# Performance work log

Hardware: AMD Instinct MI355X
Metric: run time of the kernel (lower is better)

## Reference

```python
import jax, jax.numpy as jnp
import numpy as np

N_NODES = 50000
N_EDGES = 800000
IN_CH = 128
HID = 128
OUT_CH = 10
N_GRAPHS = 64
BN_EPS = 1e-5


def _lin_init(k, fan_in, fan_out):
    k1, k2 = jax.random.split(k)
    s = 1.0 / np.sqrt(fan_in)
    W = jax.random.uniform(k1, (fan_in, fan_out), minval=-s, maxval=s, dtype=jnp.float32)
    b = jax.random.uniform(k2, (fan_out,), minval=-s, maxval=s, dtype=jnp.float32)
    return W, b


def setup_inputs() -> dict:
    key = jax.random.key(0)
    ks = jax.random.split(key, 12)
    x = jax.random.normal(ks[0], (N_NODES, IN_CH), dtype=jnp.float32)
    edge_index = jax.random.randint(ks[1], (2, N_EDGES), 0, N_NODES, dtype=jnp.int32)
    batch = jnp.sort(jax.random.randint(ks[2], (N_NODES,), 0, N_GRAPHS, dtype=jnp.int32))
    Wb0, bb0 = _lin_init(ks[3], IN_CH, HID)
    Wb1, bb1 = _lin_init(ks[4], HID, HID)
    Wa0, ba0 = _lin_init(ks[5], HID, HID)
    Wa1, ba1 = _lin_init(ks[6], HID, HID)
    Wa2, ba2 = _lin_init(ks[7], HID, HID)
    Wh0, bh0 = _lin_init(ks[8], HID, HID)
    Wh1, bh1 = _lin_init(ks[9], HID, HID)
    Wh2, bh2 = _lin_init(ks[10], HID, OUT_CH)
    ones = jnp.ones((HID,), jnp.float32)
    zeros = jnp.zeros((HID,), jnp.float32)
    return {
        'x': x, 'edge_index': edge_index, 'batch': batch, 'num_graphs': N_GRAPHS,
        'Wb0': Wb0, 'bb0': bb0, 'gb0': ones, 'betab0': zeros, 'Wb1': Wb1, 'bb1': bb1,
        'Wa0': Wa0, 'ba0': ba0, 'ga0': ones, 'bea0': zeros,
        'Wa1': Wa1, 'ba1': ba1, 'ga1': ones, 'bea1': zeros,
        'Wa2': Wa2, 'ba2': ba2,
        'Wh0': Wh0, 'bh0': bh0, 'Wh1': Wh1, 'bh1': bh1, 'Wh2': Wh2, 'bh2': bh2,
    }


def _gcn_edges(edge_index, n):
    # add self-loops, symmetric deg^{-1/2} normalization (PyG GCNConv default)
    loop = jnp.arange(n, dtype=edge_index.dtype)
    src = jnp.concatenate([edge_index[0], loop])
    dst = jnp.concatenate([edge_index[1], loop])
    deg = jax.ops.segment_sum(jnp.ones_like(dst, dtype=jnp.float32), dst, num_segments=n)
    dinv = jnp.where(deg > 0, jax.lax.rsqrt(deg), 0.0)
    return src, dst, dinv[src] * dinv[dst]


def _conv(h, W, b, src, dst, ew, n):
    hw = h @ W  # [N, F_out]
    agg = jax.ops.segment_sum(hw[src] * ew[:, None], dst, num_segments=n)
    return agg + b


def _bn(h, g, b):
    # BatchNorm1d with track_running_stats=False -> always batch statistics
    mean = jnp.mean(h, axis=0)
    var = jnp.var(h, axis=0)
    return g * (h - mean) * jax.lax.rsqrt(var + BN_EPS) + b


def _gelu(h):
    return jax.nn.gelu(h, approximate=False)


def reference(x, edge_index, batch, num_graphs,
              Wb0, bb0, gb0, betab0, Wb1, bb1,
              Wa0, ba0, ga0, bea0, Wa1, ba1, ga1, bea1, Wa2, ba2,
              Wh0, bh0, Wh1, bh1, Wh2, bh2):
    n = x.shape[0]
    src, dst, ew = _gcn_edges(edge_index, n)
    # GCN stack before (2 layers): conv -> bn -> gelu -> conv
    h = _conv(x, Wb0, bb0, src, dst, ew, n)
    h = _gelu(_bn(h, gb0, betab0))
    h = _conv(h, Wb1, bb1, src, dst, ew, n)
    # GCN stack after (3 layers)
    h = _conv(h, Wa0, ba0, src, dst, ew, n)
    h = _gelu(_bn(h, ga0, bea0))
    h = _conv(h, Wa1, ba1, src, dst, ew, n)
    h = _gelu(_bn(h, ga1, bea1))
    h = _conv(h, Wa2, ba2, src, dst, ew, n)
    # global mean pool per graph
    sums = jax.ops.segment_sum(h, batch, num_segments=num_graphs)
    cnt = jax.ops.segment_sum(jnp.ones((n,), jnp.float32), batch, num_segments=num_graphs)
    pooled = sums / jnp.maximum(cnt, 1.0)[:, None]
    # MLP head (dropout is identity in eval)
    y = _gelu(pooled @ Wh0 + bh0)
    y = _gelu(y @ Wh1 + bh1)
    return y @ Wh2 + bh2
```

## Files before the change

### kernel.cpp

```cpp
#include <hip/hip_runtime.h>
#include <math.h>

#define NN 50000
#define NE 800000
#define CH 128
#define NG 64
#define BN_EPS 1e-5f
#define POOL_CHUNK 64
#define BKT_SHIFT 9
#define NBKT ((NN + 511) >> 9)
#define PTILE 2048
#define CAP 16384

typedef short bfrag8 __attribute__((ext_vector_type(8)));
typedef float facc4 __attribute__((ext_vector_type(4)));

__device__ __forceinline__ float gelu_f(float x) {
    return 0.5f * x * (1.0f + erff(x * 0.70710678118654752440f));
}

__device__ __forceinline__ unsigned int f2bf(float f) {
    unsigned int u = __float_as_uint(f);
    return (u + 0x7FFFu + ((u >> 16) & 1u)) >> 16;
}
__device__ __forceinline__ unsigned int pack_bf2(float lo, float hi) {
    return (f2bf(hi) << 16) | f2bf(lo);
}
__device__ __forceinline__ float bf_lo(unsigned int v) { return __uint_as_float(v << 16); }
__device__ __forceinline__ float bf_hi(unsigned int v) { return __uint_as_float(v & 0xFFFF0000u); }

__global__ __launch_bounds__(256) void part_k(const int* __restrict__ ei,
                                              int* __restrict__ btail,
                                              unsigned long long* __restrict__ part) {
    __shared__ int lh[NBKT];
    __shared__ int gbase[NBKT];
    int t = threadIdx.x;
    int base = blockIdx.x * PTILE;
    if (t < NBKT) lh[t] = 0;
    __syncthreads();
    int s[8], d[8], rk[8];
    #pragma unroll
    for (int i = 0; i < 8; ++i) {
        int e = base + i * 256 + t;
        if (e < NE) {
            s[i] = ei[e];
            d[i] = ei[NE + e];
            rk[i] = atomicAdd(&lh[d[i] >> BKT_SHIFT], 1);
        }
    }
    __syncthreads();
    if (t < NBKT && lh[t]) gbase[t] = t * CAP + atomicAdd(&btail[t], lh[t]);
    __syncthreads();
    #pragma unroll
    for (int i = 0; i < 8; ++i) {
        int e = base + i * 256 + t;
        if (e < NE) {
            int b = d[i] >> BKT_SHIFT;
            part[gbase[b] + rk[i]] =
                ((unsigned long long)(unsigned int)d[i] << 32) | (unsigned int)s[i];
        }
    }
}

__global__ __launch_bounds__(256) void cscat2_k(const unsigned long long* __restrict__ part,
                                                const int* __restrict__ btail,
                                                int* __restrict__ row_ptr,
                                                int* __restrict__ row_cnt,
                                                float* __restrict__ dinv,
                                                int* __restrict__ csr_src) {
    __shared__ int cnt_l[512];
    __shared__ int off_l[512];
    __shared__ int psc[256];
    int b = blockIdx.x;
    int n0 = b << BKT_SHIFT;
    int t = threadIdx.x;
    cnt_l[t] = 0;
    cnt_l[t + 256] = 0;
    __syncthreads();
    int e0 = b * CAP, e1 = e0 + btail[b];
    for (int e = e0 + t; e < e1; e += 256) {
        int d = (int)(part[e] >> 32);
        atomicAdd(&cnt_l[d - n0], 1);
    }
    __syncthreads();
    int c0 = cnt_l[2 * t], c1 = cnt_l[2 * t + 1];
    psc[t] = c0 + c1;
    __syncthreads();
    for (int off = 1; off < 256; off <<= 1) {
        int a = (t >= off) ? psc[t - off] : 0;
        __syncthreads();
        psc[t] += a;
        __syncthreads();
    }
    int excl = (t == 0) ? 0 : psc[t - 1];
    off_l[2 * t] = excl;
    off_l[2 * t + 1] = excl + c0;
    #pragma unroll
    for (int k = 0; k < 2; ++k) {
        int ln = 2 * t + k;
        int n = n0 + ln;
        if (n < NN) {
            int c = (k == 0) ? c0 : c1;
            row_ptr[n] = e0 + off_l[ln];
            row_cnt[n] = c;
            dinv[n] = rsqrtf((float)c + 1.0f);
        }
    }
    __syncthreads();
    cnt_l[t] = 0;
    cnt_l[t + 256] = 0;
    __syncthreads();
    for (int e = e0 + t; e < e1; e += 256) {
        unsigned long long p = part[e];
        int s = (int)(unsigned int)p;
        int ld = (int)(p >> 32) - n0;
        int pos = e0 + off_l[ld] + atomicAdd(&cnt_l[ld], 1);
        csr_src[pos] = s;
    }
}

__global__ __launch_bounds__(256) void wconv_all_k(const float* __restrict__ W0,
                                                   const float* __restrict__ W1,
                                                   const float* __restrict__ W2,
                                                   const float* __restrict__ W3,
                                                   const float* __restrict__ W4,
                                                   unsigned short* __restrict__ wf) {
    int which = blockIdx.x >> 3;
    int u = (blockIdx.x & 7) * 256 + threadIdx.x;
    const float* W = (which == 0) ? W0 : (which == 1) ? W1 : (which == 2) ? W2
                   : (which == 3) ? W3 : W4;
    unsigned short* dst_wf = wf + (size_t)which * 16384;
    int nt = u >> 8, kc = (u >> 6) & 3, l = u & 63;
    int kbase = kc * 32 + (l >> 4) * 8;
    int n = nt * 16 + (l & 15);
    unsigned int p[4];
    #pragma unroll
    for (int jj = 0; jj < 4; ++jj) {
        float a = W[(kbase + 2 * jj) * 128 + n];
        float b = W[(kbase + 2 * jj + 1) * 128 + n];
        p[jj] = pack_bf2(a, b);
    }
    *(uint4*)(dst_wf + (size_t)u * 8) = make_uint4(p[0], p[1], p[2], p[3]);
}

__device__ __forceinline__ void gemm_core(unsigned short* Alds, unsigned short* Wlds,
                                          const unsigned short* wfrag, int tid,
                                          int row0, unsigned int* out16) {
    #pragma unroll
    for (int i = 0; i < 8; ++i) {
        int linear = tid + i * 256;
        ((uint4*)Wlds)[linear] = ((const uint4*)wfrag)[linear];
    }
    __syncthreads();

    const int w = tid >> 6;
    const int l = tid & 63;
    const int quad = l >> 4;
    const int m = l & 15;

    facc4 acc[8];
    #pragma unroll
    for (int nt = 0; nt < 8; ++nt) acc[nt] = (facc4){0.f, 0.f, 0.f, 0.f};

    #pragma unroll
    for (int kc = 0; kc < 4; ++kc) {
        bfrag8 a = *((const bfrag8*)(Alds + ((size_t)((w * 4 + kc) * 64 + l)) * 8));
        #pragma unroll
        for (int nt = 0; nt < 8; ++nt) {
            bfrag8 b = *((const bfrag8*)(Wlds + ((size_t)((nt * 4 + kc) * 64 + l)) * 8));
            acc[nt] = __builtin_amdgcn_mfma_f32_16x16x32_bf16(a, b, acc[nt], 0, 0, 0);
        }
    }

    #pragma unroll
    for (int nt = 0; nt < 8; ++nt) {
        #pragma unroll
        for (int r = 0; r < 4; ++r) {
            int row = row0 + w * 16 + quad * 4 + r;
            if (row < NN)
                ((unsigned short*)out16)[(size_t)row * 128 + nt * 16 + m] =
                    (unsigned short)f2bf(acc[nt][r]);
        }
    }
}

__global__ __launch_bounds__(256) void gemm_f32_k(const float* __restrict__ A,
                                                  const unsigned short* __restrict__ wfrag,
                                                  unsigned int* __restrict__ out16) {
    __shared__ unsigned short Alds[8192];
    __shared__ unsigned short Wlds[16384];
    const int tid = threadIdx.x;
    const int row0 = blockIdx.x * 64;
    #pragma unroll
    for (int i = 0; i < 4; ++i) {
        int linear = tid + i * 256;
        int r = linear >> 4;
        int g = linear & 15;
        float4 v0 = make_float4(0.f, 0.f, 0.f, 0.f);
        float4 v1 = make_float4(0.f, 0.f, 0.f, 0.f);
        if (row0 + r < NN) {
            const float4* src = (const float4*)&A[(size_t)(row0 + r) * 128 + g * 8];
            v0 = src[0];
            v1 = src[1];
        }
        int unit = (((r >> 4) * 4 + (g >> 2)) * 64) + ((g & 3) * 16) + (r & 15);
        *(uint4*)(Alds + (size_t)unit * 8) =
            make_uint4(pack_bf2(v0.x, v0.y), pack_bf2(v0.z, v0.w),
                       pack_bf2(v1.x, v1.y), pack_bf2(v1.z, v1.w));
    }
    gemm_core(Alds, Wlds, wfrag, tid, row0, out16);
}

__global__ __launch_bounds__(256) void gemm_bf16_k(const unsigned int* __restrict__ h16,
                                                   const unsigned short* __restrict__ wfrag,
                                                   const float* __restrict__ ss,
                                                   unsigned int* __restrict__ out16) {
    __shared__ unsigned short Alds[8192];
    __shared__ unsigned short Wlds[16384];
    const int tid = threadIdx.x;
    const int row0 = blockIdx.x * 64;
    #pragma unroll
    for (int i = 0; i < 4; ++i) {
        int linear = tid + i * 256;
        int r = linear >> 4;
        int g = linear & 15;
        uint4 v = make_uint4(0u, 0u, 0u, 0u);
        if (row0 + r < NN)
            v = ((const uint4*)h16)[(size_t)(row0 + r) * 16 + g];
        if (ss) {
            float4 sc0 = ((const float4*)ss)[g * 2];
            float4 sh0 = ((const float4*)ss)[32 + g * 2];
            float4 sc1 = ((const float4*)ss)[g * 2 + 1];
            float4 sh1 = ((const float4*)ss)[32 + g * 2 + 1];
            float f0 = gelu_f(bf_lo(v.x) * sc0.x + sh0.x);
            float f1 = gelu_f(bf_hi(v.x) * sc0.y + sh0.y);
            float f2 = gelu_f(bf_lo(v.y) * sc0.z + sh0.z);
            float f3 = gelu_f(bf_hi(v.y) * sc0.w + sh0.w);
            float f4 = gelu_f(bf_lo(v.z) * sc1.x + sh1.x);
            float f5 = gelu_f(bf_hi(v.z) * sc1.y + sh1.y);
            float f6 = gelu_f(bf_lo(v.w) * sc1.z + sh1.z);
            float f7 = gelu_f(bf_hi(v.w) * sc1.w + sh1.w);
            v = make_uint4(pack_bf2(f0, f1), pack_bf2(f2, f3),
                           pack_bf2(f4, f5), pack_bf2(f6, f7));
        }
        int unit = (((r >> 4) * 4 + (g >> 2)) * 64) + ((g & 3) * 16) + (r & 15);
        *(uint4*)(Alds + (size_t)unit * 8) = v;
    }
    gemm_core(Alds, Wlds, wfrag, tid, row0, out16);
}

__global__ __launch_bounds__(256) void csr_agg_k(const int* __restrict__ row_ptr,
                                                 const int* __restrict__ row_cnt,
                                                 const int* __restrict__ csr_src,
                                                 const unsigned int* __restrict__ hw16,
                                                 const float* __restrict__ bias,
                                                 const float* __restrict__ dinv,
                                                 unsigned int* __restrict__ out16) {
    int node = (blockIdx.x * 256 + threadIdx.x) >> 6;
    if (node >= NN) return;
    int lane = threadIdx.x & 63;

    float di = dinv[node];
    float sw = di * di;
    float2 b = ((const float2*)bias)[lane];
    unsigned int hs = hw16[(size_t)node * 64 + lane];
    float selfx = b.x + bf_lo(hs) * sw;
    float selfy = b.y + bf_hi(hs) * sw;

    float a0x = 0.f, a0y = 0.f, a1x = 0.f, a1y = 0.f;
    float a2x = 0.f, a2y = 0.f, a3x = 0.f, a3y = 0.f;

    int j = row_ptr[node];
    int j1 = j + row_cnt[node];
    for (; j + 7 < j1; j += 8) {
        int s[8];
        #pragma unroll
        for (int k = 0; k < 8; ++k) s[k] = csr_src[j + k];
        float w[8];
        #pragma unroll
        for (int k = 0; k < 8; ++k) w[k] = dinv[s[k]];
        unsigned int v[8];
        #pragma unroll
        for (int k = 0; k < 8; ++k) v[k] = hw16[(size_t)s[k] * 64 + lane];
        a0x += bf_lo(v[0]) * w[0] + bf_lo(v[1]) * w[1];
        a0y += bf_hi(v[0]) * w[0] + bf_hi(v[1]) * w[1];
        a1x += bf_lo(v[2]) * w[2] + bf_lo(v[3]) * w[3];
        a1y += bf_hi(v[2]) * w[2] + bf_hi(v[3]) * w[3];
        a2x += bf_lo(v[4]) * w[4] + bf_lo(v[5]) * w[5];
        a2y += bf_hi(v[4]) * w[4] + bf_hi(v[5]) * w[5];
        a3x += bf_lo(v[6]) * w[6] + bf_lo(v[7]) * w[7];
        a3y += bf_hi(v[6]) * w[6] + bf_hi(v[7]) * w[7];
    }
    for (; j + 1 < j1; j += 2) {
        int s0 = csr_src[j], s1 = csr_src[j + 1];
        float w0 = dinv[s0], w1 = dinv[s1];
        unsigned int v0 = hw16[(size_t)s0 * 64 + lane];
        unsigned int v1 = hw16[(size_t)s1 * 64 + lane];
        a0x += bf_lo(v0) * w0 + bf_lo(v1) * w1;
        a0y += bf_hi(v0) * w0 + bf_hi(v1) * w1;
    }
    if (j < j1) {
        int s = csr_src[j];
        float w = dinv[s];
        unsigned int v = hw16[(size_t)s * 64 + lane];
        a0x += bf_lo(v) * w;
        a0y += bf_hi(v) * w;
    }
    float ox = selfx + di * ((a0x + a1x) + (a2x + a3x));
    float oy = selfy + di * ((a0y + a1y) + (a2y + a3y));
    out16[(size_t)node * 64 + lane] = pack_bf2(ox, oy);
}

__global__ __launch_bounds__(256) void bn_stats_k(const unsigned int* __restrict__ h16,
                                                  float* __restrict__ sums,
                                                  int* __restrict__ counter,
                                                  const float* __restrict__ g,
                                                  const float* __restrict__ beta,
                                                  float* __restrict__ ssout) {
    int t = threadIdx.x;
    int cp = t & 63;
    int quad = t >> 6;
    float s0 = 0.f, q0 = 0.f, s1 = 0.f, q1 = 0.f;
    int r0 = blockIdx.x * 128 + quad;
    #pragma unroll 4
    for (int i = 0; i < 32; ++i) {
        int r = r0 + i * 4;
        if (r < NN) {
            unsigned int v = h16[(size_t)r * 64 + cp];
            float f0 = bf_lo(v), f1 = bf_hi(v);
            s0 += f0; q0 += f0 * f0;
            s1 += f1; q1 += f1 * f1;
        }
    }
    __shared__ float A0[256], A1[256], A2[256], A3[256];
    A0[t] = s0; A1[t] = q0; A2[t] = s1; A3[t] = q1;
    __syncthreads();
    if (t < 64) {
        float ts0 = A0[t] + A0[64 + t] + A0[128 + t] + A0[192 + t];
        float tq0 = A1[t] + A1[64 + t] + A1[128 + t] + A1[192 + t];
        float ts1 = A2[t] + A2[64 + t] + A2[128 + t] + A2[192 + t];
        float tq1 = A3[t] + A3[64 + t] + A3[128 + t] + A3[192 + t];
        atomicAdd(&sums[2 * t], ts0);
        atomicAdd(&sums[2 * t + 1], ts1);
        atomicAdd(&sums[128 + 2 * t], tq0);
        atomicAdd(&sums[129 + 2 * t], tq1);
    }
    __threadfence();
    __syncthreads();
    __shared__ int isLast;
    if (t == 0) isLast = (atomicAdd(counter, 1) == (int)gridDim.x - 1);
    __syncthreads();
    if (isLast) {
        if (t < 128) {
            float sv = atomicAdd(&sums[t], 0.f);
            float qv = atomicAdd(&sums[128 + t], 0.f);
            float mean = sv * (1.0f / NN);
            float var = qv * (1.0f / NN) - mean * mean;
            float sc = g[t] * rsqrtf(var + BN_EPS);
            ssout[t] = sc;
            ssout[128 + t] = beta[t] - mean * sc;
            sums[t] = 0.f;
            sums[128 + t] = 0.f;
        }
        if (t == 0) *counter = 0;
    }
}

__global__ __launch_bounds__(128) void pool_sum_k(const unsigned int* __restrict__ h16,
                                                  const int* __restrict__ batch,
                                                  float* __restrict__ sums) {
    int r0 = blockIdx.x * POOL_CHUNK;
    int r1 = min(r0 + POOL_CHUNK, NN);
    if (r0 >= NN) return;
    int c = threadIdx.x;
    int cp = c >> 1, hi = c & 1;
    float acc = 0.f;
    int g = batch[r0];
    for (int r = r0; r < r1; ++r) {
        int gr = batch[r];
        if (gr != g) {
            atomicAdd(&sums[g * 128 + c], acc);
            acc = 0.f;
            g = gr;
        }
        unsigned int v = h16[(size_t)r * 64 + cp];
        acc += hi ? bf_hi(v) : bf_lo(v);
    }
    atomicAdd(&sums[g * 128 + c], acc);
}

__device__ __forceinline__ int lower_bound_dev(const int* __restrict__ a, int n, int key) {
    int lo = 0, hi = n;
    while (lo < hi) {
        int mid = (lo + hi) >> 1;
        if (a[mid] < key) lo = mid + 1; else hi = mid;
    }
    return lo;
}

__global__ __launch_bounds__(128) void head_k(const float* __restrict__ psum,
                                              const int* __restrict__ batch,
                                              const float* __restrict__ W0, const float* __restrict__ b0,
                                              const float* __restrict__ W1, const float* __restrict__ b1,
                                              const float* __restrict__ W2, const float* __restrict__ b2,
                                              float* __restrict__ out) {
    __shared__ float r0[128], r1[128];
    int g = blockIdx.x, t = threadIdx.x;
    int a = lower_bound_dev(batch, NN, g);
    int b = lower_bound_dev(batch, NN, g + 1);
    float inv = 1.0f / fmaxf((float)(b - a), 1.0f);
    r0[t] = psum[g * 128 + t] * inv;
    __syncthreads();
    float acc = b0[t];
    for (int k = 0; k < 128; ++k) acc += r0[k] * W0[k * 128 + t];
    r1[t] = gelu_f(acc);
    __syncthreads();
    acc = b1[t];
    for (int k = 0; k < 128; ++k) acc += r1[k] * W1[k * 128 + t];
    float y = gelu_f(acc);
    __syncthreads();
    r0[t] = y;
    __syncthreads();
    if (t < 10) {
        acc = b2[t];
        for (int k = 0; k < 128; ++k) acc += r0[k] * W2[k * 10 + t];
        out[g * 10 + t] = acc;
    }
}

extern "C" void kernel_launch(void* const* d_in, const int* in_sizes, int n_in,
                              void* d_out, int out_size, void* d_ws, size_t ws_size,
                              hipStream_t stream) {
    const float* x      = (const float*)d_in[0];
    const int*   ei     = (const int*)d_in[1];
    const int*   batch  = (const int*)d_in[2];
    const float* Wb0    = (const float*)d_in[4];
    const float* bb0    = (const float*)d_in[5];
    const float* gb0    = (const float*)d_in[6];
    const float* betab0 = (const float*)d_in[7];
    const float* Wb1    = (const float*)d_in[8];
    const float* bb1    = (const float*)d_in[9];
    const float* Wa0    = (const float*)d_in[10];
    const float* ba0    = (const float*)d_in[11];
    const float* ga0    = (const float*)d_in[12];
    const float* bea0   = (const float*)d_in[13];
    const float* Wa1    = (const float*)d_in[14];
    const float* ba1    = (const float*)d_in[15];
    const float* ga1    = (const float*)d_in[16];
    const float* bea1   = (const float*)d_in[17];
    const float* Wa2    = (const float*)d_in[18];
    const float* ba2    = (const float*)d_in[19];
    const float* Wh0    = (const float*)d_in[20];
    const float* bh0    = (const float*)d_in[21];
    const float* Wh1    = (const float*)d_in[22];
    const float* bh1    = (const float*)d_in[23];
    const float* Wh2    = (const float*)d_in[24];
    const float* bh2    = (const float*)d_in[25];
    float* out = (float*)d_out;

    char* ws = (char*)d_ws;
    unsigned int* hw16 = (unsigned int*)ws;             ws += (size_t)NN * 64 * 4;
    unsigned int* hB   = (unsigned int*)ws;             ws += (size_t)NN * 64 * 4;
    unsigned int* hC   = (unsigned int*)ws;             ws += (size_t)NN * 64 * 4;
    float* dinv    = (float*)ws;                        ws += (size_t)NN * 4;
    int*   row_ptr = (int*)ws;                          ws += (size_t)(NN + 4) * 4;
    int*   row_cnt = (int*)ws;                          ws += (size_t)NN * 4;
    int*   csr_src = (int*)ws;                          ws += (size_t)NBKT * CAP * 4;
    unsigned long long* part = (unsigned long long*)ws; ws += (size_t)NBKT * CAP * 8;
    unsigned short* wf = (unsigned short*)ws;           ws += (size_t)5 * 16384 * 2;
    float* ssbuf   = (float*)ws;                        ws += 256 * 4;
    char* zbase = ws;
    int*   btail   = (int*)ws;                          ws += 128 * 4;
    float* bnsums  = (float*)ws;                        ws += 256 * 4;
    int*   bncnt   = (int*)ws;                          ws += 4 * 4;
    float* psum    = (float*)ws;                        ws += (size_t)NG * CH * 4;
    size_t zbytes = (size_t)(ws - zbase);

    unsigned short* wfb0 = wf;
    unsigned short* wfb1 = wf + 16384;
    unsigned short* wfa0 = wf + 2 * 16384;
    unsigned short* wfa1 = wf + 3 * 16384;
    unsigned short* wfa2 = wf + 4 * 16384;

    hipMemsetAsync(zbase, 0, zbytes, stream);
    wconv_all_k<<<40, 256, 0, stream>>>(Wb0, Wb1, Wa0, Wa1, Wa2, wf);

    part_k<<<(NE + PTILE - 1) / PTILE, 256, 0, stream>>>(ei, btail, part);
    cscat2_k<<<NBKT, 256, 0, stream>>>(part, btail, row_ptr, row_cnt, dinv, csr_src);

    auto agg = [&](const float* b, unsigned int* o) {
        csr_agg_k<<<(NN * 64 + 255) / 256, 256, 0, stream>>>(row_ptr, row_cnt, csr_src,
                                                             hw16, b, dinv, o);
    };
    auto bn_stats = [&](const unsigned int* h, const float* g, const float* beta) {
        bn_stats_k<<<(NN + 127) / 128, 256, 0, stream>>>(h, bnsums, bncnt, g, beta, ssbuf);
    };

    gemm_f32_k<<<(NN + 63) / 64, 256, 0, stream>>>(x, wfb0, hw16);
    agg(bb0, hB);
    bn_stats(hB, gb0, betab0);
    gemm_bf16_k<<<(NN + 63) / 64, 256, 0, stream>>>(hB, wfb1, ssbuf, hw16);
    agg(bb1, hC);
    gemm_bf16_k<<<(NN + 63) / 64, 256, 0, stream>>>(hC, wfa0, nullptr, hw16);
    agg(ba0, hB);
    bn_stats(hB, ga0, bea0);
    gemm_bf16_k<<<(NN + 63) / 64, 256, 0, stream>>>(hB, wfa1, ssbuf, hw16);
    agg(ba1, hC);
    bn_stats(hC, ga1, bea1);
    gemm_bf16_k<<<(NN + 63) / 64, 256, 0, stream>>>(hC, wfa2, ssbuf, hw16);
    agg(ba2, hB);

    pool_sum_k<<<(NN + POOL_CHUNK - 1) / POOL_CHUNK, 128, 0, stream>>>(hB, batch, psum);
    head_k<<<NG, 128, 0, stream>>>(psum, batch, Wh0, bh0, Wh1, bh1, Wh2, bh2, out);
}
```

Measured before the change: 592.4 us.

## Fuse BatchNorm statistics into CSR aggregation with grid-stride waves

The aggregation kernel becomes a grid-stride loop over nodes using a fixed number of blocks, and accumulates per-channel sum and sum-of-squares of its fp32 outputs, reduced in shared memory and atomically added to a global buffer. The separate BN stats kernel that re-read the bf16 activations is replaced by a tiny one-block finalize kernel. This removes one full pass over the activation tensor per BN layer, at the cost of a fixed grid that may load-balance worse across irregular node degrees. Statistics are now computed from unrounded fp32 values rather than the stored bf16 values.

```diff
diff --git a/kernel.cpp b/kernel.cpp
--- a/kernel.cpp
+++ b/kernel.cpp
@@ -11,6 +11,7 @@
 #define NBKT ((NN + 511) >> 9)
 #define PTILE 2048
 #define CAP 16384
+#define AGG_BLOCKS 2048
 
 typedef short bfrag8 __attribute__((ext_vector_type(8)));
 typedef float facc4 __attribute__((ext_vector_type(4)));
@@ -255,115 +256,110 @@
                                                  const unsigned int* __restrict__ hw16,
                                                  const float* __restrict__ bias,
                                                  const float* __restrict__ dinv,
-                                                 unsigned int* __restrict__ out16) {
-    int node = (blockIdx.x * 256 + threadIdx.x) >> 6;
-    if (node >= NN) return;
+                                                 unsigned int* __restrict__ out16,
+                                                 float* __restrict__ stats) {
     int lane = threadIdx.x & 63;
-
-    float di = dinv[node];
-    float sw = di * di;
+    int wv = threadIdx.x >> 6;
+    int wid = blockIdx.x * 4 + wv;
+    int nwaves = gridDim.x * 4;
     float2 b = ((const float2*)bias)[lane];
-    unsigned int hs = hw16[(size_t)node * 64 + lane];
-    float selfx = b.x + bf_lo(hs) * sw;
-    float selfy = b.y + bf_hi(hs) * sw;
-
-    float a0x = 0.f, a0y = 0.f, a1x = 0.f, a1y = 0.f;
-    float a2x = 0.f, a2y = 0.f, a3x = 0.f, a3y = 0.f;
-
-    int j = row_ptr[node];
-    int j1 = j + row_cnt[node];
-    for (; j + 7 < j1; j += 8) {
-        int s[8];
-        #pragma unroll
-        for (int k = 0; k < 8; ++k) s[k] = csr_src[j + k];
-        float w[8];
-        #pragma unroll
-        for (int k = 0; k < 8; ++k) w[k] = dinv[s[k]];
-        unsigned int v[8];
-        #pragma unroll
-        for (int k = 0; k < 8; ++k) v[k] = hw16[(size_t)s[k] * 64 + lane];
-        a0x += bf_lo(v[0]) * w[0] + bf_lo(v[1]) * w[1];
-        a0y += bf_hi(v[0]) * w[0] + bf_hi(v[1]) * w[1];
-        a1x += bf_lo(v[2]) * w[2] + bf_lo(v[3]) * w[3];
-        a1y += bf_hi(v[2]) * w[2] + bf_hi(v[3]) * w[3];
-        a2x += bf_lo(v[4]) * w[4] + bf_lo(v[5]) * w[5];
-        a2y += bf_hi(v[4]) * w[4] + bf_hi(v[5]) * w[5];
-        a3x += bf_lo(v[6]) * w[6] + bf_lo(v[7]) * w[7];
-        a3y += bf_hi(v[6]) * w[6] + bf_hi(v[7]) * w[7];
-    }
-    for (; j + 1 < j1; j += 2) {
-        int s0 = csr_src[j], s1 = csr_src[j + 1];
-        float w0 = dinv[s0], w1 = dinv[s1];
-        unsigned int v0 = hw16[(size_t)s0 * 64 + lane];
-        unsigned int v1 = hw16[(size_t)s1 * 64 + lane];
-        a0x += bf_lo(v0) * w0 + bf_lo(v1) * w1;
-        a0y += bf_hi(v0) * w0 + bf_hi(v1) * w1;
-    }
-    if (j < j1) {
-        int s = csr_src[j];
-        float w = dinv[s];
-        unsigned int v = hw16[(size_t)s * 64 + lane];
-        a0x += bf_lo(v) * w;
-        a0y += bf_hi(v) * w;
-    }
-    float ox = selfx + di * ((a0x + a1x) + (a2x + a3x));
-    float oy = selfy + di * ((a0y + a1y) + (a2y + a3y));
-    out16[(size_t)node * 64 + lane] = pack_bf2(ox, oy);
-}
-
-__global__ __launch_bounds__(256) void bn_stats_k(const unsigned int* __restrict__ h16,
-                                                  float* __restrict__ sums,
-                                                  int* __restrict__ counter,
-                                                  const float* __restrict__ g,
-                                                  const float* __restrict__ beta,
-                                                  float* __restrict__ ssout) {
-    int t = threadIdx.x;
-    int cp = t & 63;
-    int quad = t >> 6;
-    float s0 = 0.f, q0 = 0.f, s1 = 0.f, q1 = 0.f;
-    int r0 = blockIdx.x * 128 + quad;
-    #pragma unroll 4
-    for (int i = 0; i < 32; ++i) {
-        int r = r0 + i * 4;
-        if (r < NN) {
-            unsigned int v = h16[(size_t)r * 64 + cp];
-            float f0 = bf_lo(v), f1 = bf_hi(v);
-            s0 += f0; q0 += f0 * f0;
-            s1 += f1; q1 += f1 * f1;
-        }
-    }
-    __shared__ float A0[256], A1[256], A2[256], A3[256];
-    A0[t] = s0; A1[t] = q0; A2[t] = s1; A3[t] = q1;
-    __syncthreads();
-    if (t < 64) {
-        float ts0 = A0[t] + A0[64 + t] + A0[128 + t] + A0[192 + t];
-        float tq0 = A1[t] + A1[64 + t] + A1[128 + t] + A1[192 + t];
-        float ts1 = A2[t] + A2[64 + t] + A2[128 + t] + A2[192 + t];
-        float tq1 = A3[t] + A3[64 + t] + A3[128 + t] + A3[192 + t];
-        atomicAdd(&sums[2 * t], ts0);
-        atomicAdd(&sums[2 * t + 1], ts1);
-        atomicAdd(&sums[128 + 2 * t], tq0);
-        atomicAdd(&sums[129 + 2 * t], tq1);
-    }
-    __threadfence();
-    __syncthreads();
-    __shared__ int isLast;
-    if (t == 0) isLast = (atomicAdd(counter, 1) == (int)gridDim.x - 1);
-    __syncthreads();
-    if (isLast) {
-        if (t < 128) {
-            float sv = atomicAdd(&sums[t], 0.f);
-            float qv = atomicAdd(&sums[128 + t], 0.f);
-            float mean = sv * (1.0f / NN);
-            float var = qv * (1.0f / NN) - mean * mean;
-            float sc = g[t] * rsqrtf(var + BN_EPS);
-            ssout[t] = sc;
-            ssout[128 + t] = beta[t] - mean * sc;
-            sums[t] = 0.f;
-            sums[128 + t] = 0.f;
-        }
-        if (t == 0) *counter = 0;
-    }
+
+    float slo = 0.f, qlo = 0.f, shi = 0.f, qhi = 0.f;
+
+    for (int node = wid; node < NN; node += nwaves) {
+        float di = dinv[node];
+        float sw = di * di;
+        unsigned int hs = hw16[(size_t)node * 64 + lane];
+        float selfx = b.x + bf_lo(hs) * sw;
+        float selfy = b.y + bf_hi(hs) * sw;
+
+        float a0x = 0.f, a0y = 0.f, a1x = 0.f, a1y = 0.f;
+        float a2x = 0.f, a2y = 0.f, a3x = 0.f, a3y = 0.f;
+
+        int j = row_ptr[node];
+        int j1 = j + row_cnt[node];
+        for (; j + 7 < j1; j += 8) {
+            int s[8];
+            #pragma unroll
+            for (int k = 0; k < 8; ++k) s[k] = csr_src[j + k];
+            float w[8];
+            #pragma unroll
+            for (int k = 0; k < 8; ++k) w[k] = dinv[s[k]];
+            unsigned int v[8];
+            #pragma unroll
+            for (int k = 0; k < 8; ++k) v[k] = hw16[(size_t)s[k] * 64 + lane];
+            a0x += bf_lo(v[0]) * w[0] + bf_lo(v[1]) * w[1];
+            a0y += bf_hi(v[0]) * w[0] + bf_hi(v[1]) * w[1];
+            a1x += bf_lo(v[2]) * w[2] + bf_lo(v[3]) * w[3];
+            a1y += bf_hi(v[2]) * w[2] + bf_hi(v[3]) * w[3];
+            a2x += bf_lo(v[4]) * w[4] + bf_lo(v[5]) * w[5];
+            a2y += bf_hi(v[4]) * w[4] + bf_hi(v[5]) * w[5];
+            a3x += bf_lo(v[6]) * w[6] + bf_lo(v[7]) * w[7];
+            a3y += bf_hi(v[6]) * w[6] + bf_hi(v[7]) * w[7];
+        }
+        for (; j + 1 < j1; j += 2) {
+            int s0 = csr_src[j], s1 = csr_src[j + 1];
+            float w0 = dinv[s0], w1 = dinv[s1];
+            unsigned int v0 = hw16[(size_t)s0 * 64 + lane];
+            unsigned int v1 = hw16[(size_t)s1 * 64 + lane];
+            a0x += bf_lo(v0) * w0 + bf_lo(v1) * w1;
+            a0y += bf_hi(v0) * w0 + bf_hi(v1) * w1;
+        }
+        if (j < j1) {
+            int s = csr_src[j];
+            float w = dinv[s];
+            unsigned int v = hw16[(size_t)s * 64 + lane];
+            a0x += bf_lo(v) * w;
+            a0y += bf_hi(v) * w;
+        }
+        float ox = selfx + di * ((a0x + a1x) + (a2x + a3x));
+        float oy = selfy + di * ((a0y + a1y) + (a2y + a3y));
+        out16[(size_t)node * 64 + lane] = pack_bf2(ox, oy);
+        if (stats) {
+            slo += ox; qlo += ox * ox;
+            shi += oy; qhi += oy * oy;
+        }
+    }
+
+    if (stats) {
+        __shared__ float red[256 * 4];
+        int t = threadIdx.x;
+        red[t * 4 + 0] = slo;
+        red[t * 4 + 1] = qlo;
+        red[t * 4 + 2] = shi;
+        red[t * 4 + 3] = qhi;
+        __syncthreads();
+        if (wv == 0) {
+            float t0 = red[lane * 4 + 0] + red[(64 + lane) * 4 + 0] +
+                       red[(128 + lane) * 4 + 0] + red[(192 + lane) * 4 + 0];
+            float t1 = red[lane * 4 + 1] + red[(64 + lane) * 4 + 1] +
+                       red[(128 + lane) * 4 + 1] + red[(192 + lane) * 4 + 1];
+            float t2 = red[lane * 4 + 2] + red[(64 + lane) * 4 + 2] +
+                       red[(128 + lane) * 4 + 2] + red[(192 + lane) * 4 + 2];
+            float t3 = red[lane * 4 + 3] + red[(64 + lane) * 4 + 3] +
+                       red[(128 + lane) * 4 + 3] + red[(192 + lane) * 4 + 3];
+            atomicAdd(&stats[2 * lane], t0);
+            atomicAdd(&stats[2 * lane + 1], t2);
+            atomicAdd(&stats[128 + 2 * lane], t1);
+            atomicAdd(&stats[129 + 2 * lane], t3);
+        }
+    }
+}
+
+__global__ __launch_bounds__(128) void bn_fin_k(float* __restrict__ sums,
+                                                const float* __restrict__ g,
+                                                const float* __restrict__ beta,
+                                                float* __restrict__ ss) {
+    int c = threadIdx.x;
+    float sv = sums[c];
+    float qv = sums[128 + c];
+    float mean = sv * (1.0f / NN);
+    float var = qv * (1.0f / NN) - mean * mean;
+    float sc = g[c] * rsqrtf(var + BN_EPS);
+    ss[c] = sc;
+    ss[128 + c] = beta[c] - mean * sc;
+    sums[c] = 0.f;
+    sums[128 + c] = 0.f;
 }
 
 __global__ __launch_bounds__(128) void pool_sum_k(const unsigned int* __restrict__ h16,
@@ -472,7 +468,6 @@
     char* zbase = ws;
     int*   btail   = (int*)ws;                          ws += 128 * 4;
     float* bnsums  = (float*)ws;                        ws += 256 * 4;
-    int*   bncnt   = (int*)ws;                          ws += 4 * 4;
     float* psum    = (float*)ws;                        ws += (size_t)NG * CH * 4;
     size_t zbytes = (size_t)(ws - zbase);
 
@@ -488,27 +483,27 @@
     part_k<<<(NE + PTILE - 1) / PTILE, 256, 0, stream>>>(ei, btail, part);
     cscat2_k<<<NBKT, 256, 0, stream>>>(part, btail, row_ptr, row_cnt, dinv, csr_src);
 
-    auto agg = [&](const float* b, unsigned int* o) {
-        csr_agg_k<<<(NN * 64 + 255) / 256, 256, 0, stream>>>(row_ptr, row_cnt, csr_src,
-                                                             hw16, b, dinv, o);
+    auto agg = [&](const float* b, unsigned int* o, float* stats) {
+        csr_agg_k<<<AGG_BLOCKS, 256, 0, stream>>>(row_ptr, row_cnt, csr_src,
+                                                  hw16, b, dinv, o, stats);
     };
-    auto bn_stats = [&](const unsigned int* h, const float* g, const float* beta) {
-        bn_stats_k<<<(NN + 127) / 128, 256, 0, stream>>>(h, bnsums, bncnt, g, beta, ssbuf);
+    auto bn_fin = [&](const float* g, const float* beta) {
+        bn_fin_k<<<1, 128, 0, stream>>>(bnsums, g, beta, ssbuf);
     };
 
     gemm_f32_k<<<(NN + 63) / 64, 256, 0, stream>>>(x, wfb0, hw16);
-    agg(bb0, hB);
-    bn_stats(hB, gb0, betab0);
+    agg(bb0, hB, bnsums);
+    bn_fin(gb0, betab0);
     gemm_bf16_k<<<(NN + 63) / 64, 256, 0, stream>>>(hB, wfb1, ssbuf, hw16);
-    agg(bb1, hC);
+    agg(bb1, hC, nullptr);
     gemm_bf16_k<<<(NN + 63) / 64, 256, 0, stream>>>(hC, wfa0, nullptr, hw16);
-    agg(ba0, hB);
-    bn_stats(hB, ga0, bea0);
+    agg(ba0, hB, bnsums);
+    bn_fin(ga0, bea0);
     gemm_bf16_k<<<(NN + 63) / 64, 256, 0, stream>>>(hB, wfa1, ssbuf, hw16);
-    agg(ba1, hC);
-    bn_stats(hC, ga1, bea1);
+    agg(ba1, hC, bnsums);
+    bn_fin(ga1, bea1);
     gemm_bf16_k<<<(NN + 63) / 64, 256, 0, stream>>>(hC, wfa2, ssbuf, hw16);
-    agg(ba2, hB);
+    agg(ba2, hB, nullptr);
 
     pool_sum_k<<<(NN + POOL_CHUNK - 1) / POOL_CHUNK, 128, 0, stream>>>(hB, batch, psum);
     head_k<<<NG, 128, 0, stream>>>(psum, batch, Wh0, bh0, Wh1, bh1, Wh2, bh2, out);
```

After: 855.1 us. 1.44x slower.
